# Performance work log

Hardware: AMD Instinct MI355X
Metric: run time of the kernel (lower is better)

## Reference

```python
import jax, jax.numpy as jnp
import numpy as np
import math

B, S, D, H = 4, 2048, 1024, 16
DK = D // H  # 64


def setup_inputs() -> dict:
    key = jax.random.key(0)
    ks = jax.random.split(key, 10)
    scale = 1.0 / math.sqrt(D)
    inp = {
        "context_sequence": jax.random.normal(ks[0], (B, S, D), dtype=jnp.float32),
        "value_sequence": jax.random.normal(ks[1], (B, S, D), dtype=jnp.float32),
        "mask": jax.random.randint(ks[2], (S, S), 0, 2, dtype=jnp.int32),
        # stacked per-head projection params: [H, D, DK] weights, [H, DK] biases
        "Wq": jax.random.uniform(ks[3], (H, D, DK), jnp.float32, -scale, scale),
        "bq": jnp.zeros((H, DK), jnp.float32),
        "Wk": jax.random.uniform(ks[4], (H, D, DK), jnp.float32, -scale, scale),
        "bk": jnp.zeros((H, DK), jnp.float32),
        "Wv": jax.random.uniform(ks[5], (H, D, DK), jnp.float32, -scale, scale),
        "bv": jnp.zeros((H, DK), jnp.float32),
        "Wo": jax.random.uniform(ks[6], (D, D), jnp.float32, -scale, scale),
        "bo": jnp.zeros((D,), jnp.float32),
    }
    return inp


def reference(context_sequence, value_sequence, mask, Wq, bq, Wk, bk, Wv, bv, Wo, bo):
    # per-head projections batched over heads: [B,H,S,DK]
    Q = jnp.einsum("bsd,hdk->bhsk", context_sequence, Wq) + bq[None, :, None, :]
    K = jnp.einsum("bsd,hdk->bhsk", context_sequence, Wk) + bk[None, :, None, :]
    V = jnp.einsum("bsd,hdk->bhsk", value_sequence, Wv) + bv[None, :, None, :]
    scores = jnp.einsum("bhsk,bhtk->bhst", Q, K) / math.sqrt(DK)
    scores = jnp.where(mask[None, None, :, :] == 1, jnp.float32(-1e9), scores)
    attn = jax.nn.softmax(scores, axis=-1)
    out = jnp.einsum("bhst,bhtk->bhsk", attn, V)  # [B,H,S,DK]
    concat = out.transpose(0, 2, 1, 3).reshape(B, S, D)  # heads concatenated
    # output projection (dropout is identity in eval mode)
    return concat @ Wo.T + bo
```

## Files before the change

kernel.cpp:

```cpp
#include <hip/hip_runtime.h>
#include <hip/hip_bf16.h>

#define DEVI __device__ __forceinline__

typedef __attribute__((ext_vector_type(8))) short bf16x8;
typedef __attribute__((ext_vector_type(4))) float f32x4;
typedef unsigned short u16;
typedef unsigned long long u64;


DEVI void async16(const void* g, const void* l) {
  __builtin_amdgcn_global_load_lds(
      (const __attribute__((address_space(1))) unsigned int*)g,
      (__attribute__((address_space(3))) unsigned int*)l, 16, 0, 0);
}

DEVI u16 f2bf(float x) {
  unsigned int u = __float_as_uint(x);
  return (u16)((u + 0x7fffu + ((u >> 16) & 1u)) >> 16);
}

DEVI float fast_exp2(float x) {
#if __has_builtin(__builtin_amdgcn_exp2f)
  return __builtin_amdgcn_exp2f(x);
#else
  return exp2f(x);
#endif
}

DEVI unsigned pk_bf16(unsigned hi, unsigned lo) {
#if __has_builtin(__builtin_amdgcn_perm)
  return __builtin_amdgcn_perm(hi, lo, 0x07060302u);
#else
  return (hi & 0xffff0000u) | (lo >> 16);
#endif
}

DEVI unsigned mk2(unsigned b, int k) {
  return ((((b >> k) & 1u) ? 0u : 0x0000FFFFu) | (((b >> (k + 1)) & 1u) ? 0u : 0xFFFF0000u));
}


__global__ __launch_bounds__(256) void prep_kernel(
    const float* __restrict__ ctx, const float* __restrict__ val, const int* __restrict__ msk,
    const float* __restrict__ Wq, const float* __restrict__ Wk, const float* __restrict__ Wv,
    const float* __restrict__ Wo, const float* __restrict__ bq, const float* __restrict__ bk,
    u16* __restrict__ Xc, u16* __restrict__ Xv, u16* __restrict__ Wqt, u16* __restrict__ Wkt,
    u16* __restrict__ Wvt, u16* __restrict__ WoB, u64* __restrict__ mbits, float* __restrict__ bqk) {
  __shared__ float tile[64 * 69];
  const int blk = blockIdx.x, tid = threadIdx.x;
  if (blk < 16384) {
    const float* src = (blk < 8192) ? ctx : val;
    u16* dst = (blk < 8192) ? Xc : Xv;
    int i = (blk & 8191) * 256 + tid;
    float4 v = ((const float4*)src)[i];
    ushort4 o;
    o.x = f2bf(v.x); o.y = f2bf(v.y); o.z = f2bf(v.z); o.w = f2bf(v.w);
    ((ushort4*)dst)[i] = o;
  } else if (blk < 17408) {
    int i = (blk - 16384) * 256 + tid;
    float4 v = ((const float4*)Wo)[i];
    ushort4 o;
    o.x = f2bf(v.x); o.y = f2bf(v.y); o.z = f2bf(v.z); o.w = f2bf(v.w);
    ((ushort4*)WoB)[i] = o;
  } else if (blk < 18176) {
    int t = blk - 17408;
    int mat = t >> 8, r = t & 255, h = r >> 4, d0 = (r & 15) * 64;
    const float* Ws = (mat == 0) ? Wq : (mat == 1) ? Wk : Wv;
    u16* Wd = (mat == 0) ? Wqt : (mat == 1) ? Wkt : Wvt;
    const int dg = tid & 15, rg = tid >> 4;
#pragma unroll
    for (int i = 0; i < 4; i++) {
      int dr = rg + i * 16;
      float4 v = *(const float4*)&Ws[((size_t)(h * 1024 + d0 + dr)) * 64 + dg * 4];
      tile[dr * 69 + dg * 4 + 0] = v.x;
      tile[dr * 69 + dg * 4 + 1] = v.y;
      tile[dr * 69 + dg * 4 + 2] = v.z;
      tile[dr * 69 + dg * 4 + 3] = v.w;
    }
    __syncthreads();
#pragma unroll
    for (int i = 0; i < 4; i++) {
      int k = rg + i * 16;
      ushort4 o;
      o.x = f2bf(tile[(dg * 4 + 0) * 69 + k]);
      o.y = f2bf(tile[(dg * 4 + 1) * 69 + k]);
      o.z = f2bf(tile[(dg * 4 + 2) * 69 + k]);
      o.w = f2bf(tile[(dg * 4 + 3) * 69 + k]);
      *(ushort4*)&Wd[(size_t)(h * 64 + k) * 1024 + d0 + dg * 4] = o;
    }
  } else if (blk < 34560) {
    int gid = (blk - 18176) * 256 + tid;
    u64 bal = __ballot(msk[gid] == 1);
    if ((tid & 63) == 0) mbits[(size_t)((gid >> 6) & 31) * 2048 + (gid >> 11)] = bal;
  } else {
    int i = (blk - 34560) * 256 + tid;
    bqk[i] = (i < 1024) ? bq[i] : bk[i - 1024];
  }
}


__global__ __launch_bounds__(256) void qkv_gemm(const u16* __restrict__ Xc, const u16* __restrict__ Xv,
                                                const u16* __restrict__ Wqkt, const u16* __restrict__ Wvt,
                                                const float* __restrict__ bqk, const float* __restrict__ bvv,
                                                u16* __restrict__ QKb, u16* __restrict__ Vtg, float qscale) {
  __shared__ __align__(16) u16 As[128 * 32];
  __shared__ __align__(16) u16 Bs[128 * 32];
  const int tid = threadIdx.x;
  const int w = tid >> 6, lane = tid & 63, quad = lane >> 4, lc = lane & 15;
  const int K = 1024;
  const bool isV = blockIdx.y >= 16;
  const int m0 = blockIdx.x * 128;
  const int n0 = (isV ? (blockIdx.y - 16) : blockIdx.y) * 128;
  const u16* A  = isV ? Xv : Xc;
  const u16* Bt = isV ? Wvt : Wqkt;
  const float* bias = isV ? bvv : bqk;
  const int wrow = (w >> 1) * 64, wcol = (w & 1) * 64;
  const int srow = tid >> 2, sc = tid & 3;
  const u16* Ag = A + (size_t)(m0 + srow) * K + sc * 8;
  const u16* Bg = Bt + (size_t)(n0 + srow) * K + sc * 8;
  u16* Asw = As + w * 512;
  u16* Bsw = Bs + w * 512;

  f32x4 acc[4][4] = {};
  for (int k0 = 0; k0 < K; k0 += 32) {
    async16(Ag + k0, Asw);
    async16(Ag + k0 + (size_t)64 * K, Asw + 2048);
    async16(Bg + k0, Bsw);
    async16(Bg + k0 + (size_t)64 * K, Bsw + 2048);
    __syncthreads();
    bf16x8 af[4], bfr[4];
#pragma unroll
    for (int rt = 0; rt < 4; rt++) af[rt] = *(const bf16x8*)&As[(wrow + rt * 16 + lc) * 32 + quad * 8];
#pragma unroll
    for (int ct = 0; ct < 4; ct++) bfr[ct] = *(const bf16x8*)&Bs[(wcol + ct * 16 + lc) * 32 + quad * 8];
#pragma unroll
    for (int rt = 0; rt < 4; rt++)
#pragma unroll
      for (int ct = 0; ct < 4; ct++)
        acc[rt][ct] = __builtin_amdgcn_mfma_f32_16x16x32_bf16(af[rt], bfr[ct], acc[rt][ct], 0, 0, 0);
    __syncthreads();
  }
#pragma unroll
  for (int ct = 0; ct < 4; ct++) {
    int col = n0 + wcol + ct * 16 + lc;
    float bv = bias[col];
    float os = (!isV && col < 1024) ? qscale : 1.0f;
#pragma unroll
    for (int rt = 0; rt < 4; rt++) {
      if (isV) {
        int trow = m0 + wrow + rt * 16 + quad * 4;
        ushort4 pk;
        pk.x = f2bf(acc[rt][ct][0] + bv);
        pk.y = f2bf(acc[rt][ct][1] + bv);
        pk.z = f2bf(acc[rt][ct][2] + bv);
        pk.w = f2bf(acc[rt][ct][3] + bv);
        size_t off = ((size_t)(trow >> 11) * 1024 + col) * 2048 + (trow & 2047);
        *(ushort4*)(Vtg + off) = pk;
      } else {
#pragma unroll
        for (int r = 0; r < 4; r++) {
          int row = m0 + wrow + rt * 16 + quad * 4 + r;
          QKb[(size_t)row * 2048 + col] = f2bf((acc[rt][ct][r] + bv) * os);
        }
      }
    }
  }
}


__global__ __launch_bounds__(256, 2) void attn_kernel(const u16* __restrict__ QK, const u16* __restrict__ Vt,
                                                      const u64* __restrict__ mbits, u16* __restrict__ AO) {
  __shared__ __align__(16) u16 SM[16384];
  __shared__ uint4 Tbl[256];
  const int S = 2048, D = 1024, QS = 2048;
  const int tid = threadIdx.x, w = tid >> 6, lane = tid & 63, quad = lane >> 4, lc = lane & 15;
  const int q0 = blockIdx.x * 256;
  const int b = blockIdx.y >> 4, h = blockIdx.y & 15;
  const size_t baseq = (size_t)b * S * QS + (size_t)h * 64;
  const size_t vbase = (size_t)blockIdx.y * 64 * S;
  const int sr = lane >> 3, gch = (lane & 7) ^ sr, lx = lc & 7;

  {
    unsigned bv = (unsigned)tid;
    uint4 e;
    e.x = mk2(bv, 0); e.y = mk2(bv, 2); e.z = mk2(bv, 4); e.w = mk2(bv, 6);
    Tbl[bv] = e;
  }

#pragma unroll
  for (int i = 0; i < 8; i++) {
    const u16* g = QK + baseq + (size_t)(q0 + w * 64 + i * 8 + sr) * QS + gch * 8;
    async16(g, SM + w * 4096 + i * 512);
  }
  const int kperm = 32 * (w & 1) + 4 * (w >> 1) + 8 * (sr >> 2) + (sr & 3);
  const u16* Kg0 = QK + baseq + 1024 + (size_t)kperm * QS + gch * 8;
  const u16* Vg0 = Vt + vbase + (size_t)(w * 16 + sr) * S + gch * 8;
  __syncthreads();

  bf16x8 aq[4][2];
#pragma unroll
  for (int s = 0; s < 4; s++)
#pragma unroll
    for (int ks = 0; ks < 2; ks++)
      aq[s][ks] = *(const bf16x8*)&SM[w * 4096 + (s * 16 + lc) * 64 + (((ks * 4 + quad) ^ lx) << 3)];
  __syncthreads();

  async16(Kg0, SM + w * 1024);
  async16(Kg0 + (size_t)16 * QS, SM + w * 1024 + 512);
  async16(Vg0, SM + 8192 + w * 1024);
  async16(Vg0 + (size_t)8 * S, SM + 8192 + w * 1024 + 512);

  const u64* mptr = mbits + (size_t)(q0 + w * 64 + lc);
  const int sh8 = quad << 3;

  bf16x8 ones;
#pragma unroll
  for (int j = 0; j < 8; j++) ones[j] = (short)0x3F80;

  const f32x4 z = {};
  f32x4 acco[4][4] = {};
  f32x4 accl[4] = {};

  for (int t0 = 0; t0 < S; t0 += 64) {
    const int cur = (t0 >> 6) & 1;
    const u16* Kc = SM + cur * 4096;
    const u16* Vc = SM + 8192 + cur * 4096;
    __syncthreads();
    if (t0 + 64 < S) {
      u16* Kn = SM + (cur ^ 1) * 4096;
      u16* Vn = SM + 8192 + (cur ^ 1) * 4096;
      const u16* Kg = Kg0 + (size_t)(t0 + 64) * QS;
      const u16* Vg = Vg0 + (t0 + 64);
      async16(Kg, Kn + w * 1024);
      async16(Kg + (size_t)16 * QS, Kn + w * 1024 + 512);
      async16(Vg, Vn + w * 1024);
      async16(Vg + (size_t)8 * S, Vn + w * 1024 + 512);
    }

    u64 mw0 = mptr[(size_t)(t0 >> 6) * 2048];
    u64 mw1 = mptr[(size_t)(t0 >> 6) * 2048 + 16];
    u64 mw2 = mptr[(size_t)(t0 >> 6) * 2048 + 32];
    u64 mw3 = mptr[(size_t)(t0 >> 6) * 2048 + 48];

    bf16x8 bk0[4], bk1[4];
#pragma unroll
    for (int ct = 0; ct < 4; ct++) {
      bk0[ct] = *(const bf16x8*)&Kc[(ct * 16 + lc) * 64 + ((quad ^ lx) << 3)];
      bk1[ct] = *(const bf16x8*)&Kc[(ct * 16 + lc) * 64 + (((4 + quad) ^ lx) << 3)];
    }
    f32x4 sacc[4][4];
    __builtin_amdgcn_s_setprio(1);
#pragma unroll
    for (int s = 0; s < 4; s++)
#pragma unroll
      for (int ct = 0; ct < 4; ct++)
        sacc[s][ct] = __builtin_amdgcn_mfma_f32_16x16x32_bf16(bk0[ct], aq[s][0], z, 0, 0, 0);
#pragma unroll
    for (int s = 0; s < 4; s++)
#pragma unroll
      for (int ct = 0; ct < 4; ct++)
        sacc[s][ct] = __builtin_amdgcn_mfma_f32_16x16x32_bf16(bk1[ct], aq[s][1], sacc[s][ct], 0, 0, 0);
    __builtin_amdgcn_s_setprio(0);

    bf16x8 bv0[4], bv1[4];
#pragma unroll
    for (int ct = 0; ct < 4; ct++) {
      bv0[ct] = *(const bf16x8*)&Vc[(ct * 16 + lc) * 64 + ((quad ^ lx) << 3)];
      bv1[ct] = *(const bf16x8*)&Vc[(ct * 16 + lc) * 64 + (((4 + quad) ^ lx) << 3)];
    }

#pragma unroll
    for (int s = 0; s < 4; s++) {
      const u64 mw = (s == 0) ? mw0 : (s == 1) ? mw1 : (s == 2) ? mw2 : mw3;
      uint4 ma = Tbl[((unsigned)mw >> sh8) & 255u];
      uint4 mb = Tbl[((unsigned)(mw >> 32) >> sh8) & 255u];
      unsigned pu[4][4];
#pragma unroll
      for (int ct = 0; ct < 4; ct++)
#pragma unroll
        for (int r = 0; r < 4; r++)
          pu[ct][r] = __float_as_uint(fast_exp2(sacc[s][ct][r]));
      union { unsigned u[4]; bf16x8 v; } f0, f1;
      f0.u[0] = pk_bf16(pu[0][1], pu[0][0]) & ma.x;
      f0.u[1] = pk_bf16(pu[0][3], pu[0][2]) & ma.y;
      f0.u[2] = pk_bf16(pu[2][1], pu[2][0]) & ma.z;
      f0.u[3] = pk_bf16(pu[2][3], pu[2][2]) & ma.w;
      f1.u[0] = pk_bf16(pu[1][1], pu[1][0]) & mb.x;
      f1.u[1] = pk_bf16(pu[1][3], pu[1][2]) & mb.y;
      f1.u[2] = pk_bf16(pu[3][1], pu[3][0]) & mb.z;
      f1.u[3] = pk_bf16(pu[3][3], pu[3][2]) & mb.w;

      __builtin_amdgcn_s_setprio(1);
#pragma unroll
      for (int ct = 0; ct < 4; ct++)
        acco[s][ct] = __builtin_amdgcn_mfma_f32_16x16x32_bf16(f0.v, bv0[ct], acco[s][ct], 0, 0, 0);
      accl[s] = __builtin_amdgcn_mfma_f32_16x16x32_bf16(f0.v, ones, accl[s], 0, 0, 0);
#pragma unroll
      for (int ct = 0; ct < 4; ct++)
        acco[s][ct] = __builtin_amdgcn_mfma_f32_16x16x32_bf16(f1.v, bv1[ct], acco[s][ct], 0, 0, 0);
      accl[s] = __builtin_amdgcn_mfma_f32_16x16x32_bf16(f1.v, ones, accl[s], 0, 0, 0);
      __builtin_amdgcn_s_setprio(0);
    }
  }

#pragma unroll
  for (int s = 0; s < 4; s++)
#pragma unroll
    for (int r = 0; r < 4; r++) {
      float inv = 1.0f / accl[s][r];
      size_t row = (size_t)b * S + q0 + w * 64 + s * 16 + quad * 4 + r;
#pragma unroll
      for (int ct = 0; ct < 4; ct++)
        AO[row * D + h * 64 + ct * 16 + lc] = f2bf(acco[s][ct][r] * inv);
    }
}


__global__ __launch_bounds__(256) void out_gemm(const u16* __restrict__ A, const u16* __restrict__ Bt,
                                                const float* __restrict__ bias, float* __restrict__ C) {
  __shared__ __align__(16) u16 As[128 * 32];
  __shared__ __align__(16) u16 Bs[128 * 32];
  const int tid = threadIdx.x;
  const int w = tid >> 6, lane = tid & 63, quad = lane >> 4, lc = lane & 15;
  const int K = 1024, N = 1024;
  const int m0 = blockIdx.x * 128, n0 = blockIdx.y * 128;
  const int wrow = (w >> 1) * 64, wcol = (w & 1) * 64;
  const int srow = tid >> 2, sc = tid & 3;
  const u16* Ag = A + (size_t)(m0 + srow) * K + sc * 8;
  const u16* Bg = Bt + (size_t)(n0 + srow) * K + sc * 8;
  u16* Asw = As + w * 512;
  u16* Bsw = Bs + w * 512;

  f32x4 acc[4][4] = {};
  for (int k0 = 0; k0 < K; k0 += 32) {
    async16(Ag + k0, Asw);
    async16(Ag + k0 + (size_t)64 * K, Asw + 2048);
    async16(Bg + k0, Bsw);
    async16(Bg + k0 + (size_t)64 * K, Bsw + 2048);
    __syncthreads();
    bf16x8 af[4], bfr[4];
#pragma unroll
    for (int rt = 0; rt < 4; rt++) af[rt] = *(const bf16x8*)&As[(wrow + rt * 16 + lc) * 32 + quad * 8];
#pragma unroll
    for (int ct = 0; ct < 4; ct++) bfr[ct] = *(const bf16x8*)&Bs[(wcol + ct * 16 + lc) * 32 + quad * 8];
#pragma unroll
    for (int rt = 0; rt < 4; rt++)
#pragma unroll
      for (int ct = 0; ct < 4; ct++)
        acc[rt][ct] = __builtin_amdgcn_mfma_f32_16x16x32_bf16(af[rt], bfr[ct], acc[rt][ct], 0, 0, 0);
    __syncthreads();
  }
#pragma unroll
  for (int ct = 0; ct < 4; ct++) {
    int col = n0 + wcol + ct * 16 + lc;
    float bv = bias[col];
#pragma unroll
    for (int rt = 0; rt < 4; rt++)
#pragma unroll
      for (int r = 0; r < 4; r++) {
        int row = m0 + wrow + rt * 16 + quad * 4 + r;
        C[(size_t)row * N + col] = acc[rt][ct][r] + bv;
      }
  }
}


extern "C" void kernel_launch(void* const* d_in, const int* in_sizes, int n_in,
                              void* d_out, int out_size, void* d_ws, size_t ws_size,
                              hipStream_t stream) {
  const int B = 4, S = 2048, D = 1024;
  const float* ctx = (const float*)d_in[0];
  const float* val = (const float*)d_in[1];
  const int*   msk = (const int*)d_in[2];
  const float* Wq  = (const float*)d_in[3];
  const float* bq  = (const float*)d_in[4];
  const float* Wk  = (const float*)d_in[5];
  const float* bk  = (const float*)d_in[6];
  const float* Wv  = (const float*)d_in[7];
  const float* bv  = (const float*)d_in[8];
  const float* Wo  = (const float*)d_in[9];
  const float* bo  = (const float*)d_in[10];
  float* out = (float*)d_out;

  char* ws = (char*)d_ws;
  size_t off = 0;
  auto alloc = [&](size_t sz) { void* p = ws + off; off += (sz + 255) & ~255ULL; return p; };
  const size_t NTOK = (size_t)B * S * D;
  u16* Xc  = (u16*)alloc(NTOK * 2);
  u16* Xv  = (u16*)alloc(NTOK * 2);
  u16* Wqt = (u16*)alloc((size_t)D * D * 2);
  u16* Wkt = (u16*)alloc((size_t)D * D * 2);
  u16* Wvt = (u16*)alloc((size_t)D * D * 2);
  u16* WoB = (u16*)alloc((size_t)D * D * 2);
  u16* QKb = (u16*)alloc(NTOK * 4);
  u16* Vtg = (u16*)alloc(NTOK * 2);
  u64* mbits = (u64*)alloc((size_t)S * S / 8);
  float* bqk = (float*)alloc(2048 * 4);
  u16* AO = Xc;
  if (off > ws_size) return;

  const float qscale = 0.125f * 1.44269504088896f;

  prep_kernel<<<34568, 256, 0, stream>>>(ctx, val, msk, Wq, Wk, Wv, Wo, bq, bk,
                                         Xc, Xv, Wqt, Wkt, Wvt, WoB, mbits, bqk);

  qkv_gemm<<<dim3(B * S / 128, 24), 256, 0, stream>>>(Xc, Xv, Wqt, Wvt, bqk, bv, QKb, Vtg, qscale);

  attn_kernel<<<dim3(S / 256, B * 16), 256, 0, stream>>>(QKb, Vtg, mbits, AO);

  out_gemm<<<dim3(B * S / 128, D / 128), 256, 0, stream>>>(AO, WoB, bo, out);
}
```

Before: 326.7 us.

## Double-buffer LDS tiles in QKV and output GEMMs to overlap loads with MFMA

Both bf16 GEMM kernels now use two LDS buffers per operand. The first K-tile is prefetched before the loop, and each iteration issues the async global-to-LDS loads for the next tile right after a single barrier, then computes on the current tile. This removes the second barrier per iteration and lets global memory latency overlap with the MFMA work. LDS use per block doubles, which may lower occupancy.

```diff
diff --git a/kernel.cpp b/kernel.cpp
--- a/kernel.cpp
+++ b/kernel.cpp
@@ -104,8 +104,8 @@
                                                 const u16* __restrict__ Wqkt, const u16* __restrict__ Wvt,
                                                 const float* __restrict__ bqk, const float* __restrict__ bvv,
                                                 u16* __restrict__ QKb, u16* __restrict__ Vtg, float qscale) {
-  __shared__ __align__(16) u16 As[128 * 32];
-  __shared__ __align__(16) u16 Bs[128 * 32];
+  __shared__ __align__(16) u16 As[2][128 * 32];
+  __shared__ __align__(16) u16 Bs[2][128 * 32];
   const int tid = threadIdx.x;
   const int w = tid >> 6, lane = tid & 63, quad = lane >> 4, lc = lane & 15;
   const int K = 1024;
@@ -119,27 +119,32 @@
   const int srow = tid >> 2, sc = tid & 3;
   const u16* Ag = A + (size_t)(m0 + srow) * K + sc * 8;
   const u16* Bg = Bt + (size_t)(n0 + srow) * K + sc * 8;
-  u16* Asw = As + w * 512;
-  u16* Bsw = Bs + w * 512;
+
+  async16(Ag, As[0] + w * 512);
+  async16(Ag + (size_t)64 * K, As[0] + w * 512 + 2048);
+  async16(Bg, Bs[0] + w * 512);
+  async16(Bg + (size_t)64 * K, Bs[0] + w * 512 + 2048);
 
   f32x4 acc[4][4] = {};
   for (int k0 = 0; k0 < K; k0 += 32) {
-    async16(Ag + k0, Asw);
-    async16(Ag + k0 + (size_t)64 * K, Asw + 2048);
-    async16(Bg + k0, Bsw);
-    async16(Bg + k0 + (size_t)64 * K, Bsw + 2048);
+    const int cur = (k0 >> 5) & 1;
     __syncthreads();
+    if (k0 + 32 < K) {
+      async16(Ag + k0 + 32, As[cur ^ 1] + w * 512);
+      async16(Ag + k0 + 32 + (size_t)64 * K, As[cur ^ 1] + w * 512 + 2048);
+      async16(Bg + k0 + 32, Bs[cur ^ 1] + w * 512);
+      async16(Bg + k0 + 32 + (size_t)64 * K, Bs[cur ^ 1] + w * 512 + 2048);
+    }
     bf16x8 af[4], bfr[4];
 #pragma unroll
-    for (int rt = 0; rt < 4; rt++) af[rt] = *(const bf16x8*)&As[(wrow + rt * 16 + lc) * 32 + quad * 8];
-#pragma unroll
-    for (int ct = 0; ct < 4; ct++) bfr[ct] = *(const bf16x8*)&Bs[(wcol + ct * 16 + lc) * 32 + quad * 8];
+    for (int rt = 0; rt < 4; rt++) af[rt] = *(const bf16x8*)&As[cur][(wrow + rt * 16 + lc) * 32 + quad * 8];
+#pragma unroll
+    for (int ct = 0; ct < 4; ct++) bfr[ct] = *(const bf16x8*)&Bs[cur][(wcol + ct * 16 + lc) * 32 + quad * 8];
 #pragma unroll
     for (int rt = 0; rt < 4; rt++)
 #pragma unroll
       for (int ct = 0; ct < 4; ct++)
         acc[rt][ct] = __builtin_amdgcn_mfma_f32_16x16x32_bf16(af[rt], bfr[ct], acc[rt][ct], 0, 0, 0);
-    __syncthreads();
   }
 #pragma unroll
   for (int ct = 0; ct < 4; ct++) {
@@ -319,8 +324,8 @@
 
 __global__ __launch_bounds__(256) void out_gemm(const u16* __restrict__ A, const u16* __restrict__ Bt,
                                                 const float* __restrict__ bias, float* __restrict__ C) {
-  __shared__ __align__(16) u16 As[128 * 32];
-  __shared__ __align__(16) u16 Bs[128 * 32];
+  __shared__ __align__(16) u16 As[2][128 * 32];
+  __shared__ __align__(16) u16 Bs[2][128 * 32];
   const int tid = threadIdx.x;
   const int w = tid >> 6, lane = tid & 63, quad = lane >> 4, lc = lane & 15;
   const int K = 1024, N = 1024;
@@ -329,27 +334,32 @@
   const int srow = tid >> 2, sc = tid & 3;
   const u16* Ag = A + (size_t)(m0 + srow) * K + sc * 8;
   const u16* Bg = Bt + (size_t)(n0 + srow) * K + sc * 8;
-  u16* Asw = As + w * 512;
-  u16* Bsw = Bs + w * 512;
+
+  async16(Ag, As[0] + w * 512);
+  async16(Ag + (size_t)64 * K, As[0] + w * 512 + 2048);
+  async16(Bg, Bs[0] + w * 512);
+  async16(Bg + (size_t)64 * K, Bs[0] + w * 512 + 2048);
 
   f32x4 acc[4][4] = {};
   for (int k0 = 0; k0 < K; k0 += 32) {
-    async16(Ag + k0, Asw);
-    async16(Ag + k0 + (size_t)64 * K, Asw + 2048);
-    async16(Bg + k0, Bsw);
-    async16(Bg + k0 + (size_t)64 * K, Bsw + 2048);
+    const int cur = (k0 >> 5) & 1;
     __syncthreads();
+    if (k0 + 32 < K) {
+      async16(Ag + k0 + 32, As[cur ^ 1] + w * 512);
+      async16(Ag + k0 + 32 + (size_t)64 * K, As[cur ^ 1] + w * 512 + 2048);
+      async16(Bg + k0 + 32, Bs[cur ^ 1] + w * 512);
+      async16(Bg + k0 + 32 + (size_t)64 * K, Bs[cur ^ 1] + w * 512 + 2048);
+    }
     bf16x8 af[4], bfr[4];
 #pragma unroll
-    for (int rt = 0; rt < 4; rt++) af[rt] = *(const bf16x8*)&As[(wrow + rt * 16 + lc) * 32 + quad * 8];
-#pragma unroll
-    for (int ct = 0; ct < 4; ct++) bfr[ct] = *(const bf16x8*)&Bs[(wcol + ct * 16 + lc) * 32 + quad * 8];
+    for (int rt = 0; rt < 4; rt++) af[rt] = *(const bf16x8*)&As[cur][(wrow + rt * 16 + lc) * 32 + quad * 8];
+#pragma unroll
+    for (int ct = 0; ct < 4; ct++) bfr[ct] = *(const bf16x8*)&Bs[cur][(wcol + ct * 16 + lc) * 32 + quad * 8];
 #pragma unroll
     for (int rt = 0; rt < 4; rt++)
 #pragma unroll
       for (int ct = 0; ct < 4; ct++)
         acc[rt][ct] = __builtin_amdgcn_mfma_f32_16x16x32_bf16(af[rt], bfr[ct], acc[rt][ct], 0, 0, 0);
-    __syncthreads();
   }
 #pragma unroll
   for (int ct = 0; ct < 4; ct++) {
```

After: 318.7 us. 2.4% less time.
